# Kernel optimization log

Hardware: AMD Instinct MI355X
Metric: run time of the kernel (lower is better)

Reference implementation:

```python
import jax, jax.numpy as jnp
import numpy as np

WSCALE = 0.05  # keep qk logits in a stable range for softmax

def setup_inputs() -> dict:
    key = jax.random.key(0)
    ks = jax.random.split(key, 7)
    B, C, H, W = 8, 256, 64, 64
    d = C // 8
    x = jax.random.normal(ks[0], (B, C, H, W), dtype=jnp.float32)
    Wq = jax.random.normal(ks[1], (d, C), dtype=jnp.float32) * WSCALE
    Wk = jax.random.normal(ks[2], (d, C), dtype=jnp.float32) * WSCALE
    Wv = jax.random.normal(ks[3], (C, C), dtype=jnp.float32) * WSCALE
    bq = jnp.zeros((d,), jnp.float32)
    bk = jnp.zeros((d,), jnp.float32)
    bv = jnp.zeros((C,), jnp.float32)
    return {"x": x, "Wq": Wq, "bq": bq, "Wk": Wk, "bk": bk, "Wv": Wv, "bv": bv}

def reference(x, Wq, bq, Wk, bk, Wv, bv):
    B, C, H, W = x.shape
    N = H * W
    xf = x.reshape(B, C, N)                                  # [B,C,N]
    # 1x1 convs == per-pixel linear projections
    q = jnp.einsum('dc,bcn->bdn', Wq, xf) + bq[None, :, None]  # [B,d,N]
    k = jnp.einsum('dc,bcn->bdn', Wk, xf) + bk[None, :, None]  # [B,d,N]
    v = jnp.einsum('ec,bcn->ben', Wv, xf) + bv[None, :, None]  # [B,C,N]
    # attn[b,i,j] = q_i . k_j ; softmax over j (keys)
    attn = jax.nn.softmax(jnp.einsum('bdi,bdj->bij', q, k), axis=-1)  # [B,N,N]
    # out[b,c,i] = sum_j v[b,c,j] * attn[b,i,j]
    out = jnp.einsum('bcj,bij->bci', v, attn)                # [B,C,N]
    return out.reshape(B, C, H, W)
```

## Files before the change

### kernel.cpp

```cpp
#include <hip/hip_runtime.h>
#include <math.h>

#define NB 8
#define NC 256
#define ND 32
#define NN 4096
#define NM 320
#define LOG2E 1.44269504088896f
#define XSTR 264

typedef short short8 __attribute__((ext_vector_type(8)));
typedef float f32x4 __attribute__((ext_vector_type(4)));

#define LDS_BARRIER() asm volatile("s_waitcnt lgkmcnt(0)\ns_barrier" ::: "memory")

__device__ __forceinline__ unsigned int f2bf_u(float f) {
    return (__float_as_uint(f) + 0x8000u) >> 16;
}
__device__ __forceinline__ unsigned short f2bf(float f) {
    return (unsigned short)f2bf_u(f);
}

__global__ __launch_bounds__(256) void repack_kernel(
    const float* __restrict__ Wq, const float* __restrict__ bq,
    const float* __restrict__ Wk, const float* __restrict__ bk,
    const float* __restrict__ Wv, const float* __restrict__ bv,
    unsigned short* __restrict__ wp, float* __restrict__ bias)
{
    const int T    = blockIdx.x * 256 + threadIdx.x;
    const int j    = T & 7;
    const int lane = (T >> 3) & 63;
    const int ks   = (T >> 9) & 7;
    const int mt   = T >> 12;
    const int m = mt * 16 + (lane & 15);
    const int k = ks * 32 + ((lane >> 4) << 3) + j;
    float wv;
    if (m < 32)       wv = Wq[m * NC + k] * LOG2E;
    else if (m < 64)  wv = Wk[(m - 32) * NC + k];
    else              wv = Wv[(m - 64) * NC + k];
    wp[T] = f2bf(wv);
    if (T < NM) {
        float bb;
        if (T < 32)      bb = bq[T] * LOG2E;
        else if (T < 64) bb = bk[T - 32];
        else             bb = bv[T - 64];
        bias[T] = bb;
    }
}

__global__ __launch_bounds__(256, 4) void proj_kernel(
    const float* __restrict__ x,
    const unsigned short* __restrict__ wp,
    const float* __restrict__ bias,
    unsigned short* __restrict__ q_ws,
    unsigned short* __restrict__ k_ws,
    unsigned short* __restrict__ v_ws)
{
    __shared__ __align__(16) unsigned short xs[32 * XSTR];

    const int b  = blockIdx.x >> 7;
    const int n0 = (blockIdx.x & 127) << 5;
    const int t  = threadIdx.x;

    {
        const int n  = t & 31;
        const int cg = t >> 5;
        const float* xb = x + (size_t)b * NC * NN + n0 + n;
        #pragma unroll
        for (int it = 0; it < 8; ++it) {
            const int c = 32 * it + 4 * cg;
            const float x0 = xb[(size_t)(c + 0) * NN];
            const float x1 = xb[(size_t)(c + 1) * NN];
            const float x2 = xb[(size_t)(c + 2) * NN];
            const float x3 = xb[(size_t)(c + 3) * NN];
            uint2 pk;
            pk.x = (f2bf_u(x1) << 16) | f2bf_u(x0);
            pk.y = (f2bf_u(x3) << 16) | f2bf_u(x2);
            *(uint2*)(xs + n * XSTR + c) = pk;
        }
    }
    __syncthreads();

    const int w    = t >> 6;
    const int lane = t & 63;
    const int li = lane & 15;
    const int qd = lane >> 4;

    f32x4 acc[5][2];
    #pragma unroll
    for (int u = 0; u < 5; ++u) {
        const float bb = bias[(w + 4 * u) * 16 + li];
        acc[u][0] = (f32x4){bb, bb, bb, bb};
        acc[u][1] = (f32x4){bb, bb, bb, bb};
    }

    #pragma unroll
    for (int ks = 0; ks < 8; ++ks) {
        short8 af[2];
        #pragma unroll
        for (int mt = 0; mt < 2; ++mt)
            af[mt] = *(const short8*)(xs + (mt * 16 + li) * XSTR + ks * 32 + qd * 8);
        #pragma unroll
        for (int u = 0; u < 5; ++u) {
            const int ct = w + 4 * u;
            const short8 bf = *(const short8*)(wp + (size_t)((ct * 8 + ks) * 64 + lane) * 8);
            acc[u][0] = __builtin_amdgcn_mfma_f32_16x16x32_bf16(af[0], bf, acc[u][0], 0, 0, 0);
            acc[u][1] = __builtin_amdgcn_mfma_f32_16x16x32_bf16(af[1], bf, acc[u][1], 0, 0, 0);
        }
    }

    #pragma unroll
    for (int u = 0; u < 5; ++u) {
        const int ct = w + 4 * u;
        if (ct < 4) {
            unsigned short* dst = (ct < 2) ? q_ws : k_ws;
            const int d = (ct & 1) * 16 + li;
            #pragma unroll
            for (int mt = 0; mt < 2; ++mt)
                #pragma unroll
                for (int r = 0; r < 4; ++r) {
                    const int n = n0 + mt * 16 + 4 * qd + r;
                    dst[((size_t)b * NN + n) * ND + d] = f2bf(acc[u][mt][r]);
                }
        } else {
            const int cv = (ct - 4) * 16 + li;
            #pragma unroll
            for (int mt = 0; mt < 2; ++mt) {
                const int n = n0 + mt * 16 + 4 * qd;
                uint2 pk;
                pk.x = (f2bf_u(acc[u][mt][1]) << 16) | f2bf_u(acc[u][mt][0]);
                pk.y = (f2bf_u(acc[u][mt][3]) << 16) | f2bf_u(acc[u][mt][2]);
                *(uint2*)(v_ws + ((size_t)b * NC + cv) * NN + n) = pk;
            }
        }
    }
}

__global__ __launch_bounds__(512, 4) void attn_kernel(
    const unsigned short* __restrict__ q_ws,
    const unsigned short* __restrict__ k_ws,
    const unsigned short* __restrict__ v_ws,
    float* __restrict__ out)
{
    __shared__ __align__(16) unsigned short Pb[2][4][16 * 72];
    __shared__ float lred[8][16];

    const int b  = blockIdx.x & 7;
    const int i0 = (blockIdx.x >> 3) * 64;
    const int w    = threadIdx.x >> 6;
    const int lane = threadIdx.x & 63;
    const int li = lane & 15;
    const int qd = lane >> 4;
    const int sw = w & 3;
    const int th = w >> 2;
    const int c0 = 32 * w;

    const short8 qf = *(const short8*)(q_ws + ((size_t)b * NN + i0 + 16 * sw + li) * ND + qd * 8);
    const unsigned short* kb  = k_ws + ((size_t)b * NN + 32 * th + li) * ND + qd * 8;
    const unsigned short* vb0 = v_ws + ((size_t)b * NC + c0 + li) * NN + qd * 8;
    const unsigned short* vb1 = vb0 + (size_t)16 * NN;

    unsigned short* PA = &Pb[0][0][0];
    unsigned short* PB = &Pb[1][0][0];

    f32x4 o[4][2];
    #pragma unroll
    for (int sb = 0; sb < 4; ++sb) { o[sb][0] = (f32x4){0,0,0,0}; o[sb][1] = (f32x4){0,0,0,0}; }
    float l_loc = 0.f;
    const f32x4 z4 = {0.f, 0.f, 0.f, 0.f};

    short8 kA[2], kB[2], vA[2][2], vB[2][2];

    auto LKF = [&](int j0, short8 (&kf)[2]) {
        kf[0] = *(const short8*)(kb + (size_t)(j0     ) * ND);
        kf[1] = *(const short8*)(kb + (size_t)(j0 + 16) * ND);
    };
    auto LVF = [&](int j0, short8 (&vf)[2][2]) {
        vf[0][0] = *(const short8*)(vb0 + j0);
        vf[0][1] = *(const short8*)(vb0 + j0 + 32);
        vf[1][0] = *(const short8*)(vb1 + j0);
        vf[1][1] = *(const short8*)(vb1 + j0 + 32);
    };
    auto DOS = [&](short8 (&kf)[2], unsigned short* P) {
        unsigned short* Pw = P + sw * (16 * 72) + li * 72 + 32 * th + 4 * qd;
        #pragma unroll
        for (int tt = 0; tt < 2; ++tt) {
            const f32x4 s = __builtin_amdgcn_mfma_f32_16x16x32_bf16(kf[tt], qf, z4, 0, 0, 0);
            const float p0 = __builtin_amdgcn_exp2f(s[0]);
            const float p1 = __builtin_amdgcn_exp2f(s[1]);
            const float p2 = __builtin_amdgcn_exp2f(s[2]);
            const float p3 = __builtin_amdgcn_exp2f(s[3]);
            l_loc += (p0 + p1) + (p2 + p3);
            const unsigned u0 = __float_as_uint(p0) + 0x8000u;
            const unsigned u1 = __float_as_uint(p1) + 0x8000u;
            const unsigned u2 = __float_as_uint(p2) + 0x8000u;
            const unsigned u3 = __float_as_uint(p3) + 0x8000u;
            uint2 pk;
            pk.x = __builtin_amdgcn_perm(u1, u0, 0x07060302u);
            pk.y = __builtin_amdgcn_perm(u3, u2, 0x07060302u);
            *(uint2*)(Pw + 16 * tt) = pk;
        }
    };
    auto DOPV = [&](const unsigned short* P, short8 (&vf)[2][2]) {
        #pragma unroll
        for (int sb = 0; sb < 4; ++sb) {
            const unsigned short* Pr = P + sb * (16 * 72) + li * 72 + qd * 8;
            const short8 pf0 = *(const short8*)(Pr);
            const short8 pf1 = *(const short8*)(Pr + 32);
            o[sb][0] = __builtin_amdgcn_mfma_f32_16x16x32_bf16(vf[0][0], pf0, o[sb][0], 0, 0, 0);
            o[sb][0] = __builtin_amdgcn_mfma_f32_16x16x32_bf16(vf[0][1], pf1, o[sb][0], 0, 0, 0);
            o[sb][1] = __builtin_amdgcn_mfma_f32_16x16x32_bf16(vf[1][0], pf0, o[sb][1], 0, 0, 0);
            o[sb][1] = __builtin_amdgcn_mfma_f32_16x16x32_bf16(vf[1][1], pf1, o[sb][1], 0, 0, 0);
        }
    };

    LKF(0, kA); LVF(0, vA);
    DOS(kA, PA);
    LKF(64, kB);
    LDS_BARRIER();

    int j = 0;
    #pragma unroll 1
    for (int it = 0; it < 31; ++it) {
        LVF(j + 64, vB);
        DOPV(PA, vA);
        DOS(kB, PB);
        LKF(j + 128, kA);
        LDS_BARRIER();
        LVF(j + 128, vA);
        DOPV(PB, vB);
        DOS(kA, PA);
        LKF(j + 192, kB);
        LDS_BARRIER();
        j += 128;
    }
    LVF(4032, vB);
    DOPV(PA, vA);
    DOS(kB, PB);
    LDS_BARRIER();
    DOPV(PB, vB);

    l_loc += __shfl_xor(l_loc, 16, 64);
    l_loc += __shfl_xor(l_loc, 32, 64);
    if (lane < 16) lred[w][li] = l_loc;
    __syncthreads();
    float linv[4];
    #pragma unroll
    for (int sb = 0; sb < 4; ++sb)
        linv[sb] = 1.0f / (lred[sb][li] + lred[sb + 4][li]);

    #pragma unroll
    for (int sb = 0; sb < 4; ++sb)
        #pragma unroll
        for (int ct = 0; ct < 2; ++ct) {
            const int c = c0 + ct * 16 + qd * 4;
            float* op = out + ((size_t)b * NC + c) * NN + i0 + 16 * sb + li;
            #pragma unroll
            for (int r = 0; r < 4; ++r)
                op[(size_t)r * NN] = o[sb][ct][r] * linv[sb];
        }
}

extern "C" void kernel_launch(void* const* d_in, const int* in_sizes, int n_in,
                              void* d_out, int out_size, void* d_ws, size_t ws_size,
                              hipStream_t stream) {
    const float* x  = (const float*)d_in[0];
    const float* Wq = (const float*)d_in[1];
    const float* bq = (const float*)d_in[2];
    const float* Wk = (const float*)d_in[3];
    const float* bk = (const float*)d_in[4];
    const float* Wv = (const float*)d_in[5];
    const float* bv = (const float*)d_in[6];
    float* out = (float*)d_out;

    unsigned short* q_ws = (unsigned short*)d_ws;
    unsigned short* k_ws = q_ws + (size_t)NB * NN * ND;
    unsigned short* v_ws = k_ws + (size_t)NB * NN * ND;
    unsigned short* wp   = v_ws + (size_t)NB * NC * NN;
    float*          bias = (float*)(wp + (size_t)NM * NC);

    repack_kernel<<<NM * NC / 256, 256, 0, stream>>>(Wq, bq, Wk, bk, Wv, bv, wp, bias);
    proj_kernel<<<NB * (NN / 32), 256, 0, stream>>>(x, wp, bias, q_ws, k_ws, v_ws);
    attn_kernel<<<NB * (NN / 64), 512, 0, stream>>>(q_ws, k_ws, v_ws, out);
}
```

Baseline: 246.2 us.

## Halve attention block to 4 waves, each computing full score tile and 64 channels

```diff
diff --git a/kernel.cpp b/kernel.cpp
--- a/kernel.cpp
+++ b/kernel.cpp
@@ -136,14 +136,14 @@
     }
 }
 
-__global__ __launch_bounds__(512, 4) void attn_kernel(
+__global__ __launch_bounds__(256, 2) void attn_kernel(
     const unsigned short* __restrict__ q_ws,
     const unsigned short* __restrict__ k_ws,
     const unsigned short* __restrict__ v_ws,
     float* __restrict__ out)
 {
     __shared__ __align__(16) unsigned short Pb[2][4][16 * 72];
-    __shared__ float lred[8][16];
+    __shared__ float lred[4][16];
 
     const int b  = blockIdx.x & 7;
     const int i0 = (blockIdx.x >> 3) * 64;
@@ -151,40 +151,44 @@
     const int lane = threadIdx.x & 63;
     const int li = lane & 15;
     const int qd = lane >> 4;
-    const int sw = w & 3;
-    const int th = w >> 2;
-    const int c0 = 32 * w;
+    const int sw = w;
+    const int c0 = 64 * w;
 
     const short8 qf = *(const short8*)(q_ws + ((size_t)b * NN + i0 + 16 * sw + li) * ND + qd * 8);
-    const unsigned short* kb  = k_ws + ((size_t)b * NN + 32 * th + li) * ND + qd * 8;
-    const unsigned short* vb0 = v_ws + ((size_t)b * NC + c0 + li) * NN + qd * 8;
-    const unsigned short* vb1 = vb0 + (size_t)16 * NN;
+    const unsigned short* kb = k_ws + ((size_t)b * NN + li) * ND + qd * 8;
+    const unsigned short* vb = v_ws + ((size_t)b * NC + c0 + li) * NN + qd * 8;
 
     unsigned short* PA = &Pb[0][0][0];
     unsigned short* PB = &Pb[1][0][0];
 
-    f32x4 o[4][2];
-    #pragma unroll
-    for (int sb = 0; sb < 4; ++sb) { o[sb][0] = (f32x4){0,0,0,0}; o[sb][1] = (f32x4){0,0,0,0}; }
+    f32x4 o[4][4];
+    #pragma unroll
+    for (int sb = 0; sb < 4; ++sb)
+        #pragma unroll
+        for (int ct = 0; ct < 4; ++ct)
+            o[sb][ct] = (f32x4){0.f, 0.f, 0.f, 0.f};
     float l_loc = 0.f;
     const f32x4 z4 = {0.f, 0.f, 0.f, 0.f};
 
-    short8 kA[2], kB[2], vA[2][2], vB[2][2];
-
-    auto LKF = [&](int j0, short8 (&kf)[2]) {
-        kf[0] = *(const short8*)(kb + (size_t)(j0     ) * ND);
-        kf[1] = *(const short8*)(kb + (size_t)(j0 + 16) * ND);
-    };
-    auto LVF = [&](int j0, short8 (&vf)[2][2]) {
-        vf[0][0] = *(const short8*)(vb0 + j0);
-        vf[0][1] = *(const short8*)(vb0 + j0 + 32);
-        vf[1][0] = *(const short8*)(vb1 + j0);
-        vf[1][1] = *(const short8*)(vb1 + j0 + 32);
-    };
-    auto DOS = [&](short8 (&kf)[2], unsigned short* P) {
-        unsigned short* Pw = P + sw * (16 * 72) + li * 72 + 32 * th + 4 * qd;
-        #pragma unroll
-        for (int tt = 0; tt < 2; ++tt) {
+    short8 kA[4], kB[4], vA[4][2], vB[4][2];
+
+    auto LKF = [&](int j0, short8 (&kf)[4]) {
+        #pragma unroll
+        for (int tt = 0; tt < 4; ++tt)
+            kf[tt] = *(const short8*)(kb + (size_t)(j0 + 16 * tt) * ND);
+    };
+    auto LVF = [&](int j0, short8 (&vf)[4][2]) {
+        #pragma unroll
+        for (int t = 0; t < 4; ++t) {
+            const unsigned short* vt = vb + (size_t)(16 * t) * NN;
+            vf[t][0] = *(const short8*)(vt + j0);
+            vf[t][1] = *(const short8*)(vt + j0 + 32);
+        }
+    };
+    auto DOS = [&](short8 (&kf)[4], unsigned short* P) {
+        unsigned short* Pw = P + sw * (16 * 72) + li * 72 + 4 * qd;
+        #pragma unroll
+        for (int tt = 0; tt < 4; ++tt) {
             const f32x4 s = __builtin_amdgcn_mfma_f32_16x16x32_bf16(kf[tt], qf, z4, 0, 0, 0);
             const float p0 = __builtin_amdgcn_exp2f(s[0]);
             const float p1 = __builtin_amdgcn_exp2f(s[1]);
@@ -201,16 +205,17 @@
             *(uint2*)(Pw + 16 * tt) = pk;
         }
     };
-    auto DOPV = [&](const unsigned short* P, short8 (&vf)[2][2]) {
+    auto DOPV = [&](const unsigned short* P, short8 (&vf)[4][2]) {
         #pragma unroll
         for (int sb = 0; sb < 4; ++sb) {
             const unsigned short* Pr = P + sb * (16 * 72) + li * 72 + qd * 8;
             const short8 pf0 = *(const short8*)(Pr);
             const short8 pf1 = *(const short8*)(Pr + 32);
-            o[sb][0] = __builtin_amdgcn_mfma_f32_16x16x32_bf16(vf[0][0], pf0, o[sb][0], 0, 0, 0);
-            o[sb][0] = __builtin_amdgcn_mfma_f32_16x16x32_bf16(vf[0][1], pf1, o[sb][0], 0, 0, 0);
-            o[sb][1] = __builtin_amdgcn_mfma_f32_16x16x32_bf16(vf[1][0], pf0, o[sb][1], 0, 0, 0);
-            o[sb][1] = __builtin_amdgcn_mfma_f32_16x16x32_bf16(vf[1][1], pf1, o[sb][1], 0, 0, 0);
+            #pragma unroll
+            for (int ct = 0; ct < 4; ++ct) {
+                o[sb][ct] = __builtin_amdgcn_mfma_f32_16x16x32_bf16(vf[ct][0], pf0, o[sb][ct], 0, 0, 0);
+                o[sb][ct] = __builtin_amdgcn_mfma_f32_16x16x32_bf16(vf[ct][1], pf1, o[sb][ct], 0, 0, 0);
+            }
         }
     };
 
@@ -223,20 +228,20 @@
     #pragma unroll 1
     for (int it = 0; it < 31; ++it) {
         LVF(j + 64, vB);
+        DOS(kB, PB);
         DOPV(PA, vA);
-        DOS(kB, PB);
         LKF(j + 128, kA);
         LDS_BARRIER();
         LVF(j + 128, vA);
+        DOS(kA, PA);
         DOPV(PB, vB);
-        DOS(kA, PA);
         LKF(j + 192, kB);
         LDS_BARRIER();
         j += 128;
     }
     LVF(4032, vB);
+    DOS(kB, PB);
     DOPV(PA, vA);
-    DOS(kB, PB);
     LDS_BARRIER();
     DOPV(PB, vB);
 
@@ -247,12 +252,12 @@
     float linv[4];
     #pragma unroll
     for (int sb = 0; sb < 4; ++sb)
-        linv[sb] = 1.0f / (lred[sb][li] + lred[sb + 4][li]);
+        linv[sb] = 1.0f / lred[sb][li];
 
     #pragma unroll
     for (int sb = 0; sb < 4; ++sb)
         #pragma unroll
-        for (int ct = 0; ct < 2; ++ct) {
+        for (int ct = 0; ct < 4; ++ct) {
             const int c = c0 + ct * 16 + qd * 4;
             float* op = out + ((size_t)b * NC + c) * NN + i0 + 16 * sb + li;
             #pragma unroll
@@ -281,5 +286,5 @@
 
     repack_kernel<<<NM * NC / 256, 256, 0, stream>>>(Wq, bq, Wk, bk, Wv, bv, wp, bias);
     proj_kernel<<<NB * (NN / 32), 256, 0, stream>>>(x, wp, bias, q_ws, k_ws, v_ws);
-    attn_kernel<<<NB * (NN / 64), 512, 0, stream>>>(q_ws, k_ws, v_ws, out);
-}
+    attn_kernel<<<NB * (NN / 64), 256, 0, stream>>>(q_ws, k_ws, v_ws, out);
+}
```

Measured after the change: 252.3 us. +2.5%, slower.
